# Kernel tuning notes

Measured on AMD Instinct MI355X. Metric: run time of the kernel, lower is better.

Reference implementation:

```python
import jax, jax.numpy as jnp
import numpy as np
import math

KH = KW = 3
STRIDE = 1
PAD = 1
DIL = 1
C_IN = 256
C_OUT = 256
RANK = 32
BATCH = 16
H = W = 56


def setup_inputs() -> dict:
    key = jax.random.key(0)
    kx, kg, kh_, kb = jax.random.split(key, 4)
    x = jax.random.normal(kx, (BATCH, C_IN, H, W), dtype=jnp.float32)
    k2 = KH * KW
    bg = 1.0 / math.sqrt(C_IN)
    bh = 1.0 / math.sqrt(RANK)
    G = jax.random.uniform(kg, (k2, RANK, C_IN), minval=-bg, maxval=bg, dtype=jnp.float32)
    Hm = jax.random.uniform(kh_, (k2, C_OUT, RANK), minval=-bh, maxval=bh, dtype=jnp.float32)
    bias = jax.random.uniform(kb, (C_OUT,), minval=-bg, maxval=bg, dtype=jnp.float32)
    return {"x": x, "G": G, "Hm": Hm, "bias": bias}


def reference(x, G, Hm, bias):
    # Low-rank conv: per kernel position k, project patch through G[k] (rank) then H[k] (out),
    # then MEAN over the k2 positions (matches the original's .mean(dim=0)).
    b, c, h, w = x.shape
    h_out = (h + 2 * PAD - DIL * (KH - 1) - 1) // STRIDE + 1
    w_out = (h + 2 * PAD - DIL * (KW - 1) - 1) // STRIDE + 1  # original uses h here; square input
    xp = jnp.pad(x, ((0, 0), (0, 0), (PAD, PAD), (PAD, PAD)))
    acc = jnp.zeros((b, Hm.shape[1], h_out, w_out), dtype=x.dtype)
    for i in range(KH):
        for j in range(KW):
            k = i * KW + j
            # strided patch view for kernel offset (i, j): [b, c, h_out, w_out]
            patch = xp[:, :,
                       i * DIL:i * DIL + (h_out - 1) * STRIDE + 1:STRIDE,
                       j * DIL:j * DIL + (w_out - 1) * STRIDE + 1:STRIDE]
            t = jnp.einsum('bchw,rc->brhw', patch, G[k])      # rank projection
            acc = acc + jnp.einsum('brhw,or->bohw', t, Hm[k])  # out projection
    out = acc / (KH * KW) + bias[None, :, None, None]
    return out
```

## Files before the change

kernel.cpp:

```cpp
#include <hip/hip_runtime.h>
#include <stdint.h>


#define BATCH 16
#define CIN   256
#define COUT  256
#define RANK  32
#define HH    56
#define WW    56
#define SP    (HH*WW)
#define YP    58
#define XP    58
#define PCELL (YP*XP)
#define PLANE (BATCH*PCELL)

typedef __bf16 bf16x8 __attribute__((ext_vector_type(8)));
typedef float  f32x4  __attribute__((ext_vector_type(4)));

#define OFF_T9 0
#define OFF_GB 31002624
#define OFF_HB (OFF_GB + 147456)

#define RING_U4 (9 * 16 * 228 * 4)
#define PREP_N  (147456 + RING_U4)

__device__ __forceinline__ uint16_t bfbits(float f) {
  __bf16 h = (__bf16)f;
  return __builtin_bit_cast(uint16_t, h);
}

__global__ __launch_bounds__(256) void k_prep(const float* __restrict__ G,
                                              const float* __restrict__ Hm,
                                              uint16_t* __restrict__ G_bf,
                                              uint16_t* __restrict__ Hm_bf,
                                              uint16_t* __restrict__ T9) {
  int i = blockIdx.x * 256 + threadIdx.x;
  if (i < 73728)  { G_bf[i] = bfbits(G[i]); return; }
  if (i < 147456) { Hm_bf[i - 73728] = bfbits(Hm[i - 73728]); return; }
  int j = i - 147456;
  if (j >= RING_U4) return;
  int v = j & 3, cell = j >> 2;
  int tb = cell / 228, c = cell % 228;
  int y, xx;
  if      (c < 58)  { y = 0;       xx = c;       }
  else if (c < 116) { y = 57;      xx = c - 58;  }
  else if (c < 172) { y = c - 115; xx = 0;       }
  else              { y = c - 171; xx = 57;      }
  uint16_t* base = T9 + ((size_t)tb * PCELL + y * XP + xx) * 32;
  uint4 z; z.x = z.y = z.z = z.w = 0u;
  ((uint4*)base)[v] = z;
}

__global__ __launch_bounds__(384, 3) void k_fused1(const float* __restrict__ x,
                                                   const uint16_t* __restrict__ G_bf,
                                                   uint16_t* __restrict__ T9) {
  __shared__ uint16_t xs[32 * 264];
  const int tid = threadIdx.x;
  const int wave = tid >> 6, lane = tid & 63;
  const int q = lane >> 4, t = lane & 15;

  bf16x8 A[3][8];
  {
    const uint16_t* gb = G_bf + (size_t)(wave * 48 + t) * CIN + q * 8;
#pragma unroll
    for (int i = 0; i < 3; ++i)
#pragma unroll
      for (int ks = 0; ks < 8; ++ks)
        A[i][ks] = *(const bf16x8*)(gb + (size_t)i * 16 * CIN + ks * 32);
  }

#pragma unroll 1
  for (int rep = 0; rep < 2; ++rep) {
    const int item = blockIdx.x * 2 + rep;
    const int b = item / 98, ch = item - b * 98;

#pragma unroll 1
    for (int u = tid; u < 1024; u += 384) {
      const int s = u & 31, cg = u >> 5;
      const float* xr = x + ((size_t)(b * CIN + cg * 8)) * SP + ch * 32 + s;
      bf16x8 v;
#pragma unroll
      for (int e = 0; e < 8; ++e)
        ((__bf16*)&v)[e] = (__bf16)xr[(size_t)e * SP];
      *(bf16x8*)&xs[s * 264 + cg * 8] = v;
    }
    __syncthreads();

#pragma unroll 1
    for (int nt = 0; nt < 2; ++nt) {
      bf16x8 Bf[8];
#pragma unroll
      for (int ks = 0; ks < 8; ++ks)
        Bf[ks] = *(const bf16x8*)&xs[(nt * 16 + t) * 264 + ks * 32 + q * 8];

      f32x4 acc[3];
#pragma unroll
      for (int i = 0; i < 3; ++i) acc[i] = (f32x4){0.f, 0.f, 0.f, 0.f};
#pragma unroll
      for (int ks = 0; ks < 8; ++ks)
#pragma unroll
        for (int i = 0; i < 3; ++i)
          acc[i] = __builtin_amdgcn_mfma_f32_16x16x32_bf16(A[i][ks], Bf[ks], acc[i], 0, 0, 0);

      const int p = ch * 32 + nt * 16 + t;
      const int h = p / WW, w = p - (p / WW) * WW;
      const size_t cellbase = ((size_t)b * PCELL + (h + 1) * XP + (w + 1)) * 32;
#pragma unroll
      for (int i = 0; i < 3; ++i) {
        const int kr0 = wave * 48 + i * 16 + q * 4;
        const int tap = kr0 >> 5, r = kr0 & 31;
        uint2 pv;
        pv.x = (uint32_t)bfbits(acc[i][0]) | ((uint32_t)bfbits(acc[i][1]) << 16);
        pv.y = (uint32_t)bfbits(acc[i][2]) | ((uint32_t)bfbits(acc[i][3]) << 16);
        *(uint2*)(T9 + (size_t)tap * PLANE * 32 + cellbase + r) = pv;
      }
    }
    __syncthreads();
  }
}

__global__ __launch_bounds__(512, 4) void k_stage2(const uint16_t* __restrict__ T9,
                                                   const uint16_t* __restrict__ Hm_bf,
                                                   const float* __restrict__ bias,
                                                   float* __restrict__ out) {
  const int wave = threadIdx.x >> 6, lane = threadIdx.x & 63;
  const int q = lane >> 4, t = lane & 15;

  bf16x8 Bf[9][2];
  float bv[2];
#pragma unroll
  for (int j = 0; j < 2; ++j) {
    const int o = wave * 32 + j * 16 + t;
    bv[j] = bias[o];
#pragma unroll
    for (int tap = 0; tap < 9; ++tap)
      Bf[tap][j] = *(const bf16x8*)(Hm_bf + ((size_t)(tap * COUT + o)) * RANK + q * 8);
  }

#pragma unroll 1
  for (int it = 0; it < 4; ++it) {
    const int mt = blockIdx.x * 4 + it;
    const int p0 = mt * 16;
    const int b = p0 / SP, s0 = p0 - b * SP;
    const int sa = s0 + t;
    const int ha = sa / WW, wa = sa - ha * WW;
    const uint16_t* abase = T9 + ((size_t)(b * PCELL + ha * XP + wa)) * 32 + q * 8;

    f32x4 acc[2];
    acc[0] = (f32x4){0.f, 0.f, 0.f, 0.f};
    acc[1] = (f32x4){0.f, 0.f, 0.f, 0.f};
#pragma unroll
    for (int tap = 0; tap < 9; ++tap) {
      const int di = tap / 3, dj = tap % 3;
      bf16x8 af = *(const bf16x8*)(abase + (size_t)tap * PLANE * 32 + (di * XP + dj) * 32);
      acc[0] = __builtin_amdgcn_mfma_f32_16x16x32_bf16(af, Bf[tap][0], acc[0], 0, 0, 0);
      acc[1] = __builtin_amdgcn_mfma_f32_16x16x32_bf16(af, Bf[tap][1], acc[1], 0, 0, 0);
    }

    const int sd = s0 + q * 4;
#pragma unroll
    for (int j = 0; j < 2; ++j) {
      const int o = wave * 32 + j * 16 + t;
      f32x4 v = acc[j] * (1.0f / 9.0f) + bv[j];
      *(f32x4*)(out + ((size_t)(b * COUT + o)) * SP + sd) = v;
    }
  }
}

extern "C" void kernel_launch(void* const* d_in, const int* in_sizes, int n_in,
                              void* d_out, int out_size, void* d_ws, size_t ws_size,
                              hipStream_t stream) {
  const float* x    = (const float*)d_in[0];
  const float* G    = (const float*)d_in[1];
  const float* Hm   = (const float*)d_in[2];
  const float* bias = (const float*)d_in[3];
  float* out = (float*)d_out;
  char* ws = (char*)d_ws;

  uint16_t* T9    = (uint16_t*)(ws + OFF_T9);
  uint16_t* G_bf  = (uint16_t*)(ws + OFF_GB);
  uint16_t* Hm_bf = (uint16_t*)(ws + OFF_HB);

  k_prep<<<PREP_N / 256, 256, 0, stream>>>(G, Hm, G_bf, Hm_bf, T9);
  k_fused1<<<784, 384, 0, stream>>>(x, G_bf, T9);
  k_stage2<<<784, 512, 0, stream>>>(T9, Hm_bf, bias, out);
}
```

Baseline: 157.4 us.

## Load x fragments directly from global in stage1, drop LDS staging

Stage1 now has each wave read its bf16 B-fragments for 16-pixel tiles straight from global memory and convert them in registers. This replaces the cooperative LDS transpose and its barriers, so every one of the six waves re-reads the same x data through cache rather than sharing it. Stage2's tile ordering changes from consecutive tiles per block to a stride of the grid size across iterations. The intent is to remove LDS traffic and syncs and to spread memory accesses differently.

Result: slower. 257.8 us (+63.8%).

```diff
diff --git a/kernel.cpp b/kernel.cpp
--- a/kernel.cpp
+++ b/kernel.cpp
@@ -51,10 +51,9 @@
   ((uint4*)base)[v] = z;
 }
 
-__global__ __launch_bounds__(384, 3) void k_fused1(const float* __restrict__ x,
+__global__ __launch_bounds__(384, 3) void k_stage1(const float* __restrict__ x,
                                                    const uint16_t* __restrict__ G_bf,
                                                    uint16_t* __restrict__ T9) {
-  __shared__ uint16_t xs[32 * 264];
   const int tid = threadIdx.x;
   const int wave = tid >> 6, lane = tid & 63;
   const int q = lane >> 4, t = lane & 15;
@@ -70,52 +69,42 @@
   }
 
 #pragma unroll 1
-  for (int rep = 0; rep < 2; ++rep) {
-    const int item = blockIdx.x * 2 + rep;
-    const int b = item / 98, ch = item - b * 98;
+  for (int pt = 0; pt < 4; ++pt) {
+    const int tile = blockIdx.x * 4 + pt;
+    const int p0 = tile * 16;
+    const int b = p0 / SP, s0 = p0 - b * SP;
+    const float* xb = x + ((size_t)b * CIN + q * 8) * SP + s0 + t;
 
-#pragma unroll 1
-    for (int u = tid; u < 1024; u += 384) {
-      const int s = u & 31, cg = u >> 5;
-      const float* xr = x + ((size_t)(b * CIN + cg * 8)) * SP + ch * 32 + s;
-      bf16x8 v;
+    f32x4 acc[3];
 #pragma unroll
-      for (int e = 0; e < 8; ++e)
-        ((__bf16*)&v)[e] = (__bf16)xr[(size_t)e * SP];
-      *(bf16x8*)&xs[s * 264 + cg * 8] = v;
+    for (int i = 0; i < 3; ++i) acc[i] = (f32x4){0.f, 0.f, 0.f, 0.f};
+
+#pragma unroll
+    for (int ks = 0; ks < 8; ++ks) {
+      const float* xc = xb + (size_t)(ks * 32) * SP;
+      float tmp[8];
+#pragma unroll
+      for (int e = 0; e < 8; ++e) tmp[e] = xc[(size_t)e * SP];
+      bf16x8 Bf;
+#pragma unroll
+      for (int e = 0; e < 8; ++e) ((__bf16*)&Bf)[e] = (__bf16)tmp[e];
+#pragma unroll
+      for (int i = 0; i < 3; ++i)
+        acc[i] = __builtin_amdgcn_mfma_f32_16x16x32_bf16(A[i][ks], Bf, acc[i], 0, 0, 0);
     }
-    __syncthreads();
 
-#pragma unroll 1
-    for (int nt = 0; nt < 2; ++nt) {
-      bf16x8 Bf[8];
+    const int p = s0 + t;
+    const int h = p / WW, w = p - (p / WW) * WW;
+    const size_t cellbase = ((size_t)b * PCELL + (h + 1) * XP + (w + 1)) * 32;
 #pragma unroll
-      for (int ks = 0; ks < 8; ++ks)
-        Bf[ks] = *(const bf16x8*)&xs[(nt * 16 + t) * 264 + ks * 32 + q * 8];
-
-      f32x4 acc[3];
-#pragma unroll
-      for (int i = 0; i < 3; ++i) acc[i] = (f32x4){0.f, 0.f, 0.f, 0.f};
-#pragma unroll
-      for (int ks = 0; ks < 8; ++ks)
-#pragma unroll
-        for (int i = 0; i < 3; ++i)
-          acc[i] = __builtin_amdgcn_mfma_f32_16x16x32_bf16(A[i][ks], Bf[ks], acc[i], 0, 0, 0);
-
-      const int p = ch * 32 + nt * 16 + t;
-      const int h = p / WW, w = p - (p / WW) * WW;
-      const size_t cellbase = ((size_t)b * PCELL + (h + 1) * XP + (w + 1)) * 32;
-#pragma unroll
-      for (int i = 0; i < 3; ++i) {
-        const int kr0 = wave * 48 + i * 16 + q * 4;
-        const int tap = kr0 >> 5, r = kr0 & 31;
-        uint2 pv;
-        pv.x = (uint32_t)bfbits(acc[i][0]) | ((uint32_t)bfbits(acc[i][1]) << 16);
-        pv.y = (uint32_t)bfbits(acc[i][2]) | ((uint32_t)bfbits(acc[i][3]) << 16);
-        *(uint2*)(T9 + (size_t)tap * PLANE * 32 + cellbase + r) = pv;
-      }
+    for (int i = 0; i < 3; ++i) {
+      const int kr0 = wave * 48 + i * 16 + q * 4;
+      const int tap = kr0 >> 5, r = kr0 & 31;
+      uint2 pv;
+      pv.x = (uint32_t)bfbits(acc[i][0]) | ((uint32_t)bfbits(acc[i][1]) << 16);
+      pv.y = (uint32_t)bfbits(acc[i][2]) | ((uint32_t)bfbits(acc[i][3]) << 16);
+      *(uint2*)(T9 + (size_t)tap * PLANE * 32 + cellbase + r) = pv;
     }
-    __syncthreads();
   }
 }
 
@@ -139,7 +128,7 @@
 
 #pragma unroll 1
   for (int it = 0; it < 4; ++it) {
-    const int mt = blockIdx.x * 4 + it;
+    const int mt = blockIdx.x + it * 784;
     const int p0 = mt * 16;
     const int b = p0 / SP, s0 = p0 - b * SP;
     const int sa = s0 + t;
@@ -182,6 +171,6 @@
   uint16_t* Hm_bf = (uint16_t*)(ws + OFF_HB);
 
   k_prep<<<PREP_N / 256, 256, 0, stream>>>(G, Hm, G_bf, Hm_bf, T9);
-  k_fused1<<<784, 384, 0, stream>>>(x, G_bf, T9);
+  k_stage1<<<784, 384, 0, stream>>>(x, G_bf, T9);
   k_stage2<<<784, 512, 0, stream>>>(T9, Hm_bf, bias, out);
 }
```
